# Optimization experiments

Hardware: AMD Instinct MI355X
Metric: run time of the kernel (lower is better)

The kernel has to match this reference:

```python
import jax, jax.numpy as jnp
import numpy as np

TAU = 0.03        # self.tau
EPS = 0.65       # args.epsilon
EPS2 = 0.4       # args.epsilon2 (trimap)
LOGIT_T = 0.07    # logits temperature


def _l2norm(x, axis):
    # torch F.normalize: x / max(||x||, 1e-12)
    n = jnp.sqrt(jnp.sum(x * x, axis=axis, keepdims=True))
    return x / jnp.maximum(n, 1e-12)


def setup_inputs() -> dict:
    key = jax.random.key(0)
    k1, k2 = jax.random.split(key)
    img = jax.random.normal(k1, (256, 512, 14, 14), dtype=jnp.float32)
    aud = jax.random.normal(k2, (256, 512), dtype=jnp.float32)
    return {"img": img, "aud": aud}


def reference(img, aud):
    # img: [B, C, H, W] backbone vision features; aud: [B, C] pooled audio features
    B = img.shape[0]
    img = _l2norm(img, axis=1)
    aud = _l2norm(aud, axis=1)

    # A: paired audio-visual correlation map [B, 1, H, W]
    A = jnp.einsum('nchw,nc->nhw', img, aud)[:, None]
    # A0: full cross-pair correlation maps [B, B, H, W] (n = image idx, m = audio idx)
    A0 = jnp.einsum('nchw,mc->nmhw', img, aud)
    # AdaptiveMaxPool2d((1,1)) -> max over spatial dims -> [B, B]
    A0_ref = jnp.max(A0, axis=(2, 3))

    Pos = jax.nn.sigmoid((A - EPS) / TAU)           # [B, 1, H, W]
    Pos2 = jax.nn.sigmoid((A - EPS2) / TAU)         # trimap branch
    Neg = 1.0 - Pos2
    Pos_all = jax.nn.sigmoid((A0 - EPS) / TAU)      # [B, B, H, W]

    mask = 1.0 - 100.0 * jnp.eye(B, dtype=img.dtype)
    # gated weighted-mean pooling over spatial dims
    sim = (Pos_all * A0).sum(axis=(2, 3)) / Pos_all.sum(axis=(2, 3)) * mask   # [B, B]
    sim1 = (Pos * A).sum(axis=(2, 3)) / Pos.sum(axis=(2, 3))                  # [B, 1]
    sim2 = (Neg * A).sum(axis=(2, 3)) / Neg.sum(axis=(2, 3))                  # [B, 1]

    logits = jnp.concatenate((sim1, sim, sim2), axis=1) / LOGIT_T             # [B, B+2]
    return (A, logits, Pos, Neg, A0_ref)
```

## Files before the change

### kernel.cpp

```cpp
#include <hip/hip_runtime.h>
#include <math.h>

typedef _Float16 half8 __attribute__((ext_vector_type(8)));
typedef float f32x4 __attribute__((ext_vector_type(4)));

#define RLT (1.0f/0.07f)


__device__ __forceinline__ void gll16(const void* g, void* l) {
    __builtin_amdgcn_global_load_lds(
        (const __attribute__((address_space(1))) void*)g,
        (__attribute__((address_space(3))) void*)l, 16, 0, 0);
}

__global__ __launch_bounds__(256) void prep_aud_pk(const float* __restrict__ aud,
                                                   _Float16* __restrict__ aud_pk) {
    int m = blockIdx.x, t = threadIdx.x;
    float a0 = aud[m * 512 + t];
    float a1 = aud[m * 512 + 256 + t];
    float s = a0 * a0 + a1 * a1;
    #pragma unroll
    for (int off = 32; off; off >>= 1) s += __shfl_down(s, off, 64);
    __shared__ float wsum[4];
    __shared__ float rns;
    if ((t & 63) == 0) wsum[t >> 6] = s;
    __syncthreads();
    if (t == 0) rns = 1.0f / fmaxf(sqrtf(wsum[0] + wsum[1] + wsum[2] + wsum[3]), 1e-12f);
    __syncthreads();
    float rn = rns;
    int c0 = t, c1 = t + 256;
    aud_pk[(c0 >> 3) * 2048 + m * 8 + (c0 & 7)] = (_Float16)(a0 * rn);
    aud_pk[(c1 >> 3) * 2048 + m * 8 + (c1 & 7)] = (_Float16)(a1 * rn);
}

__global__ __launch_bounds__(512) void av_mfma2(const float* __restrict__ img,
                                                const _Float16* __restrict__ aud_pk,
                                                float* __restrict__ out) {
    const int n = blockIdx.x;
    const int tid = threadIdx.x;
    const int w = tid >> 6, l = tid & 63;
    const int q = w & 3;
    const int hh = w >> 2;
    const int HT = hh ? 6 : 7;

    __shared__ _Float16 __align__(16) Abuf[2][4][208][8];
    __shared__ _Float16 __align__(16) Bbuf[2][4][256][8];
    __shared__ float rnorm_s[208];
    __shared__ float nrm_parts[2][196];
    __shared__ float red_max[2][256], red_sw[2][256], red_swa[2][256];
    __shared__ float diag_parts[2][4][4];

    if (tid < 96) {
        int b = tid / 48, rem = tid % 48, kg = rem / 12, row = 196 + rem % 12;
        *(float4*)&Abuf[b][kg][row][0] = make_float4(0.f, 0.f, 0.f, 0.f);
    }

    const float* imgn = img + (size_t)n * (512 * 196);
    const bool act = tid < 392;
    const int p   = act ? tid / 196 : 0;
    const int hws = act ? tid % 196 : 0;
    float nrm = 0.f;
    float av[16];

    #define STAGE_B(t, buf)                                                        \
        do {                                                                       \
            const _Float16* g0 = aud_pk + (((size_t)(t) * 1024 + w * 64 + l) << 3);\
            _Float16* l0 = &Bbuf[buf][0][0][0] + ((w * 64) << 3);                  \
            gll16(g0, l0);                                                         \
            gll16(g0 + 4096, l0 + 4096);                                           \
        } while (0)

    #define STAGE_A(buf)                                                           \
        do {                                                                       \
            if (act) {                                                             \
                half8 h0, h1;                                                      \
                _Pragma("unroll")                                                  \
                for (int i = 0; i < 8; i++) {                                      \
                    h0[i] = (_Float16)av[i];                                       \
                    h1[i] = (_Float16)av[8 + i];                                   \
                    nrm += av[i] * av[i] + av[8 + i] * av[8 + i];                   \
                }                                                                  \
                *(half8*)&Abuf[buf][2 * p][hws][0]     = h0;                       \
                *(half8*)&Abuf[buf][2 * p + 1][hws][0] = h1;                       \
            }                                                                      \
        } while (0)

    STAGE_B(0, 0);
    if (act) {
        const float* src = imgn + (size_t)(p * 16) * 196 + hws;
        #pragma unroll
        for (int i = 0; i < 16; i++) av[i] = src[i * 196];
    }
    STAGE_A(0);
    __syncthreads();

    f32x4 acc[7][4];
    #pragma unroll
    for (int ht = 0; ht < 7; ht++)
        #pragma unroll
        for (int mt = 0; mt < 4; mt++)
            acc[ht][mt] = (f32x4){0.f, 0.f, 0.f, 0.f};

    const int aoff = (l >> 4) * 1664 + (hh * 112 + (l & 15)) * 8;
    const int boff = (l >> 4) * 2048 + (q * 64 + (l & 15)) * 8;

    for (int t = 0; t < 16; t++) {
        const int cur = t & 1, nb = cur ^ 1;
        const bool more = t < 15;
        if (more) {
            STAGE_B(t + 1, nb);
            if (act) {
                const float* src = imgn + (size_t)(32 * (t + 1) + p * 16) * 196 + hws;
                #pragma unroll
                for (int i = 0; i < 16; i++) av[i] = src[i * 196];
            }
        }
        {
            const _Float16* Ab = &Abuf[cur][0][0][0];
            const _Float16* Bb = &Bbuf[cur][0][0][0];
            half8 bfrag[4];
            #pragma unroll
            for (int mt = 0; mt < 4; mt++) bfrag[mt] = *(const half8*)(Bb + boff + mt * 128);
            half8 afrag[7];
            #pragma unroll
            for (int ht = 0; ht < 7; ht++)
                if (ht < HT) afrag[ht] = *(const half8*)(Ab + aoff + ht * 128);
            #pragma unroll
            for (int ht = 0; ht < 7; ht++)
                if (ht < HT)
                    #pragma unroll
                    for (int mt = 0; mt < 4; mt++)
                        acc[ht][mt] = __builtin_amdgcn_mfma_f32_16x16x32_f16(
                            afrag[ht], bfrag[mt], acc[ht][mt], 0, 0, 0);
        }
        if (more) STAGE_A(nb);
        __syncthreads();
    }

    if (act) nrm_parts[p][hws] = nrm;
    __syncthreads();
    if (tid < 208) {
        float v = 0.f;
        if (tid < 196) {
            float s = nrm_parts[0][tid] + nrm_parts[1][tid];
            v = 1.0f / fmaxf(sqrtf(s), 1e-12f);
        }
        rnorm_s[tid] = v;
    }
    __syncthreads();

    float mx[4], sw[4], swa[4];
    #pragma unroll
    for (int mt = 0; mt < 4; mt++) { mx[mt] = -1e30f; sw[mt] = 0.f; swa[mt] = 0.f; }
    float s1n = 0.f, s1d = 0.f, s2n = 0.f, s2d = 0.f;
    const int dmt = (n >> 4) & 3, dq = n >> 6, dl = n & 15;
    const bool isdiag = (q == dq) && ((l & 15) == dl);

    #pragma unroll
    for (int ht = 0; ht < 7; ht++) {
        if (ht < HT) {
            int rowb = hh * 112 + ht * 16 + ((l >> 4) << 2);
            #pragma unroll
            for (int r = 0; r < 4; r++) {
                int hw = rowb + r;
                float rn = rnorm_s[hw];
                bool valid = hw < 196;
                #pragma unroll
                for (int mt = 0; mt < 4; mt++) {
                    float a0 = acc[ht][mt][r] * rn;
                    if (valid) {
                        float wg = 1.0f / (1.0f + __expf((0.65f - a0) * (1.0f / 0.03f)));
                        mx[mt]  = fmaxf(mx[mt], a0);
                        sw[mt] += wg;
                        swa[mt] += wg * a0;
                        if (isdiag && mt == dmt) {
                            out[n * 196 + hw] = a0;
                            out[116224 + n * 196 + hw] = wg;
                            float p2 = 1.0f / (1.0f + __expf((0.40f - a0) * (1.0f / 0.03f)));
                            float ng = 1.0f - p2;
                            out[166400 + n * 196 + hw] = ng;
                            s1n += wg * a0; s1d += wg;
                            s2n += ng * a0; s2d += ng;
                        }
                    }
                }
            }
        }
    }

    #pragma unroll
    for (int mt = 0; mt < 4; mt++) {
        float m1 = mx[mt], v1 = sw[mt], v2 = swa[mt];
        m1 = fmaxf(m1, __shfl_xor(m1, 16, 64)); v1 += __shfl_xor(v1, 16, 64); v2 += __shfl_xor(v2, 16, 64);
        m1 = fmaxf(m1, __shfl_xor(m1, 32, 64)); v1 += __shfl_xor(v1, 32, 64); v2 += __shfl_xor(v2, 32, 64);
        if (l < 16) {
            int m = q * 64 + mt * 16 + l;
            red_max[hh][m] = m1; red_sw[hh][m] = v1; red_swa[hh][m] = v2;
        }
    }
    if (isdiag) {
        diag_parts[hh][l >> 4][0] = s1n;
        diag_parts[hh][l >> 4][1] = s1d;
        diag_parts[hh][l >> 4][2] = s2n;
        diag_parts[hh][l >> 4][3] = s2d;
    }
    __syncthreads();

    if (tid < 256) {
        int m = tid;
        float mxv = fmaxf(red_max[0][m], red_max[1][m]);
        float num = red_swa[0][m] + red_swa[1][m];
        float den = red_sw[0][m] + red_sw[1][m];
        float sim = num / den;
        if (m == n) sim *= -99.0f;
        out[50176 + n * 258 + 1 + m] = sim * RLT;
        out[216576 + n * 256 + m] = mxv;
        if (m == n) {
            float t1n = 0.f, t1d = 0.f, t2n = 0.f, t2d = 0.f;
            #pragma unroll
            for (int h2 = 0; h2 < 2; h2++)
                #pragma unroll
                for (int g = 0; g < 4; g++) {
                    t1n += diag_parts[h2][g][0]; t1d += diag_parts[h2][g][1];
                    t2n += diag_parts[h2][g][2]; t2d += diag_parts[h2][g][3];
                }
            out[50176 + n * 258]       = (t1n / t1d) * RLT;
            out[50176 + n * 258 + 257] = (t2n / t2d) * RLT;
        }
    }
}

extern "C" void kernel_launch(void* const* d_in, const int* in_sizes, int n_in,
                              void* d_out, int out_size, void* d_ws, size_t ws_size,
                              hipStream_t stream) {
    const float* img = (const float*)d_in[0];
    const float* aud = (const float*)d_in[1];
    float* out = (float*)d_out;
    _Float16* aud_pk = (_Float16*)d_ws;

    prep_aud_pk<<<256, 256, 0, stream>>>(aud, aud_pk);
    av_mfma2<<<256, 512, 0, stream>>>(img, aud_pk, out);
}
```

Measured before the change: 48.58 us.

## Split each image's spatial range across two blocks with a separate reduction kernel

Each image is now handled by two workgroups, each covering 98 of the 196 spatial positions, so the grid grows from 256 to 512 blocks and fills more compute units on the GPU. Partial max, weighted sums and diagonal terms are written to workspace, and a new small kernel combines them to produce the logits and pooled maxima. This costs an extra kernel launch and some workspace traffic. Each block also reads the full audio tile, so B-operand staging is duplicated across the two halves.

Measured after the change: 42.78 us. 11.9% less time.

```diff
diff --git a/kernel.cpp b/kernel.cpp
--- a/kernel.cpp
+++ b/kernel.cpp
@@ -33,75 +33,84 @@
     aud_pk[(c1 >> 3) * 2048 + m * 8 + (c1 & 7)] = (_Float16)(a1 * rn);
 }
 
-__global__ __launch_bounds__(512) void av_mfma2(const float* __restrict__ img,
-                                                const _Float16* __restrict__ aud_pk,
-                                                float* __restrict__ out) {
-    const int n = blockIdx.x;
+__global__ __launch_bounds__(512, 4) void av_split(const float* __restrict__ img,
+                                                   const _Float16* __restrict__ aud_pk,
+                                                   float* __restrict__ out,
+                                                   float* __restrict__ pmax,
+                                                   float* __restrict__ psw,
+                                                   float* __restrict__ pswa,
+                                                   float* __restrict__ pdiag) {
+    const int bid = blockIdx.x;
+    const int n = bid >> 1, half = bid & 1;
     const int tid = threadIdx.x;
     const int w = tid >> 6, l = tid & 63;
     const int q = w & 3;
-    const int hh = w >> 2;
-    const int HT = hh ? 6 : 7;
-
-    __shared__ _Float16 __align__(16) Abuf[2][4][208][8];
+    const int hg = w >> 2;
+    const int HT = hg ? 3 : 4;
+
+    __shared__ _Float16 __align__(16) Abuf[2][4][112][8];
     __shared__ _Float16 __align__(16) Bbuf[2][4][256][8];
-    __shared__ float rnorm_s[208];
-    __shared__ float nrm_parts[2][196];
+    __shared__ float nrm_parts[4][98];
+    __shared__ float rnorm_s[112];
     __shared__ float red_max[2][256], red_sw[2][256], red_swa[2][256];
     __shared__ float diag_parts[2][4][4];
 
-    if (tid < 96) {
-        int b = tid / 48, rem = tid % 48, kg = rem / 12, row = 196 + rem % 12;
+    if (tid < 112) {
+        int b = tid / 56, rem = tid % 56, kg = rem / 14, row = 98 + rem % 14;
         *(float4*)&Abuf[b][kg][row][0] = make_float4(0.f, 0.f, 0.f, 0.f);
     }
 
     const float* imgn = img + (size_t)n * (512 * 196);
     const bool act = tid < 392;
-    const int p   = act ? tid / 196 : 0;
-    const int hws = act ? tid % 196 : 0;
+    const int p   = act ? tid / 98 : 0;
+    const int hwl = act ? tid % 98 : 0;
+    const int g   = half * 98 + hwl;
     float nrm = 0.f;
-    float av[16];
-
-    #define STAGE_B(t, buf)                                                        \
-        do {                                                                       \
-            const _Float16* g0 = aud_pk + (((size_t)(t) * 1024 + w * 64 + l) << 3);\
-            _Float16* l0 = &Bbuf[buf][0][0][0] + ((w * 64) << 3);                  \
-            gll16(g0, l0);                                                         \
-            gll16(g0 + 4096, l0 + 4096);                                           \
+    float av[8];
+
+    #define STAGE_B(t, buf)                                                         \
+        do {                                                                        \
+            const _Float16* g0 = aud_pk + (((size_t)(t) * 1024 + tid) << 3);        \
+            _Float16* l0 = &Bbuf[buf][0][0][0] + ((w * 64) << 3);                   \
+            gll16(g0, l0);                                                          \
+            gll16(g0 + 4096, l0 + 4096);                                            \
         } while (0)
 
-    #define STAGE_A(buf)                                                           \
-        do {                                                                       \
-            if (act) {                                                             \
-                half8 h0, h1;                                                      \
-                _Pragma("unroll")                                                  \
-                for (int i = 0; i < 8; i++) {                                      \
-                    h0[i] = (_Float16)av[i];                                       \
-                    h1[i] = (_Float16)av[8 + i];                                   \
-                    nrm += av[i] * av[i] + av[8 + i] * av[8 + i];                   \
-                }                                                                  \
-                *(half8*)&Abuf[buf][2 * p][hws][0]     = h0;                       \
-                *(half8*)&Abuf[buf][2 * p + 1][hws][0] = h1;                       \
-            }                                                                      \
+    #define LOAD_A(t)                                                               \
+        do {                                                                        \
+            if (act) {                                                              \
+                const float* src = imgn + ((size_t)(32 * (t) + p * 8)) * 196 + g;   \
+                _Pragma("unroll")                                                   \
+                for (int i = 0; i < 8; i++) av[i] = src[i * 196];                   \
+            }                                                                       \
         } while (0)
 
+    #define STAGE_A(buf)                                                            \
+        do {                                                                        \
+            if (act) {                                                              \
+                half8 h0;                                                           \
+                _Pragma("unroll")                                                   \
+                for (int i = 0; i < 8; i++) {                                       \
+                    h0[i] = (_Float16)av[i];                                        \
+                    nrm += av[i] * av[i];                                           \
+                }                                                                   \
+                *(half8*)&Abuf[buf][p][hwl][0] = h0;                                \
+            }                                                                       \
+        } while (0)
+
     STAGE_B(0, 0);
-    if (act) {
-        const float* src = imgn + (size_t)(p * 16) * 196 + hws;
-        #pragma unroll
-        for (int i = 0; i < 16; i++) av[i] = src[i * 196];
-    }
+    LOAD_A(0);
     STAGE_A(0);
     __syncthreads();
 
-    f32x4 acc[7][4];
-    #pragma unroll
-    for (int ht = 0; ht < 7; ht++)
+    f32x4 acc[4][4];
+    #pragma unroll
+    for (int ht = 0; ht < 4; ht++)
         #pragma unroll
         for (int mt = 0; mt < 4; mt++)
             acc[ht][mt] = (f32x4){0.f, 0.f, 0.f, 0.f};
 
-    const int aoff = (l >> 4) * 1664 + (hh * 112 + (l & 15)) * 8;
+    const int aoff = (l >> 4) * 896  + (hg * 64 + (l & 15)) * 8;
     const int boff = (l >> 4) * 2048 + (q * 64 + (l & 15)) * 8;
 
     for (int t = 0; t < 16; t++) {
@@ -109,11 +118,7 @@
         const bool more = t < 15;
         if (more) {
             STAGE_B(t + 1, nb);
-            if (act) {
-                const float* src = imgn + (size_t)(32 * (t + 1) + p * 16) * 196 + hws;
-                #pragma unroll
-                for (int i = 0; i < 16; i++) av[i] = src[i * 196];
-            }
+            LOAD_A(t + 1);
         }
         {
             const _Float16* Ab = &Abuf[cur][0][0][0];
@@ -121,12 +126,12 @@
             half8 bfrag[4];
             #pragma unroll
             for (int mt = 0; mt < 4; mt++) bfrag[mt] = *(const half8*)(Bb + boff + mt * 128);
-            half8 afrag[7];
-            #pragma unroll
-            for (int ht = 0; ht < 7; ht++)
+            half8 afrag[4];
+            #pragma unroll
+            for (int ht = 0; ht < 4; ht++)
                 if (ht < HT) afrag[ht] = *(const half8*)(Ab + aoff + ht * 128);
             #pragma unroll
-            for (int ht = 0; ht < 7; ht++)
+            for (int ht = 0; ht < 4; ht++)
                 if (ht < HT)
                     #pragma unroll
                     for (int mt = 0; mt < 4; mt++)
@@ -137,14 +142,13 @@
         __syncthreads();
     }
 
-    if (act) nrm_parts[p][hws] = nrm;
-    __syncthreads();
-    if (tid < 208) {
+    if (act) nrm_parts[p][hwl] = nrm;
+    __syncthreads();
+    if (tid < 112) {
         float v = 0.f;
-        if (tid < 196) {
-            float s = nrm_parts[0][tid] + nrm_parts[1][tid];
-            v = 1.0f / fmaxf(sqrtf(s), 1e-12f);
-        }
+        if (tid < 98)
+            v = 1.0f / fmaxf(sqrtf(nrm_parts[0][tid] + nrm_parts[1][tid] +
+                                   nrm_parts[2][tid] + nrm_parts[3][tid]), 1e-12f);
         rnorm_s[tid] = v;
     }
     __syncthreads();
@@ -157,14 +161,15 @@
     const bool isdiag = (q == dq) && ((l & 15) == dl);
 
     #pragma unroll
-    for (int ht = 0; ht < 7; ht++) {
+    for (int ht = 0; ht < 4; ht++) {
         if (ht < HT) {
-            int rowb = hh * 112 + ht * 16 + ((l >> 4) << 2);
+            int rowb = hg * 64 + ht * 16 + ((l >> 4) << 2);
             #pragma unroll
             for (int r = 0; r < 4; r++) {
-                int hw = rowb + r;
-                float rn = rnorm_s[hw];
-                bool valid = hw < 196;
+                int row = rowb + r;
+                float rn = rnorm_s[row];
+                bool valid = row < 98;
+                int hw = half * 98 + row;
                 #pragma unroll
                 for (int mt = 0; mt < 4; mt++) {
                     float a0 = acc[ht][mt][r] * rn;
@@ -195,38 +200,54 @@
         m1 = fmaxf(m1, __shfl_xor(m1, 32, 64)); v1 += __shfl_xor(v1, 32, 64); v2 += __shfl_xor(v2, 32, 64);
         if (l < 16) {
             int m = q * 64 + mt * 16 + l;
-            red_max[hh][m] = m1; red_sw[hh][m] = v1; red_swa[hh][m] = v2;
+            red_max[hg][m] = m1; red_sw[hg][m] = v1; red_swa[hg][m] = v2;
         }
     }
     if (isdiag) {
-        diag_parts[hh][l >> 4][0] = s1n;
-        diag_parts[hh][l >> 4][1] = s1d;
-        diag_parts[hh][l >> 4][2] = s2n;
-        diag_parts[hh][l >> 4][3] = s2d;
+        diag_parts[hg][l >> 4][0] = s1n;
+        diag_parts[hg][l >> 4][1] = s1d;
+        diag_parts[hg][l >> 4][2] = s2n;
+        diag_parts[hg][l >> 4][3] = s2d;
     }
     __syncthreads();
 
     if (tid < 256) {
         int m = tid;
-        float mxv = fmaxf(red_max[0][m], red_max[1][m]);
-        float num = red_swa[0][m] + red_swa[1][m];
-        float den = red_sw[0][m] + red_sw[1][m];
-        float sim = num / den;
-        if (m == n) sim *= -99.0f;
-        out[50176 + n * 258 + 1 + m] = sim * RLT;
-        out[216576 + n * 256 + m] = mxv;
-        if (m == n) {
-            float t1n = 0.f, t1d = 0.f, t2n = 0.f, t2d = 0.f;
-            #pragma unroll
-            for (int h2 = 0; h2 < 2; h2++)
-                #pragma unroll
-                for (int g = 0; g < 4; g++) {
-                    t1n += diag_parts[h2][g][0]; t1d += diag_parts[h2][g][1];
-                    t2n += diag_parts[h2][g][2]; t2d += diag_parts[h2][g][3];
-                }
-            out[50176 + n * 258]       = (t1n / t1d) * RLT;
-            out[50176 + n * 258 + 257] = (t2n / t2d) * RLT;
-        }
+        int base = (n * 2 + half) * 256 + m;
+        pmax[base] = fmaxf(red_max[0][m], red_max[1][m]);
+        psw[base]  = red_sw[0][m] + red_sw[1][m];
+        pswa[base] = red_swa[0][m] + red_swa[1][m];
+    }
+    if (tid < 4) {
+        float s = 0.f;
+        #pragma unroll
+        for (int h2 = 0; h2 < 2; h2++)
+            #pragma unroll
+            for (int lg = 0; lg < 4; lg++)
+                s += diag_parts[h2][lg][tid];
+        pdiag[(n * 2 + half) * 4 + tid] = s;
+    }
+    #undef STAGE_B
+    #undef LOAD_A
+    #undef STAGE_A
+}
+
+__global__ __launch_bounds__(256) void av_final(const float* __restrict__ pmax,
+                                                const float* __restrict__ psw,
+                                                const float* __restrict__ pswa,
+                                                const float* __restrict__ pdiag,
+                                                float* __restrict__ out) {
+    int n = blockIdx.x, m = threadIdx.x;
+    int b0 = (n * 2) * 256 + m, b1 = (n * 2 + 1) * 256 + m;
+    float mx = fmaxf(pmax[b0], pmax[b1]);
+    float sim = (pswa[b0] + pswa[b1]) / (psw[b0] + psw[b1]);
+    if (m == n) sim *= -99.0f;
+    out[50176 + n * 258 + 1 + m] = sim * RLT;
+    out[216576 + n * 256 + m] = mx;
+    if (m == n) {
+        const float* d = pdiag + n * 8;
+        out[50176 + n * 258]       = ((d[0] + d[4]) / (d[1] + d[5])) * RLT;
+        out[50176 + n * 258 + 257] = ((d[2] + d[6]) / (d[3] + d[7])) * RLT;
     }
 }
 
@@ -236,8 +257,15 @@
     const float* img = (const float*)d_in[0];
     const float* aud = (const float*)d_in[1];
     float* out = (float*)d_out;
+
     _Float16* aud_pk = (_Float16*)d_ws;
+    float* wsf   = (float*)d_ws;
+    float* pmax  = wsf + 32768;
+    float* psw   = pmax + 131072;
+    float* pswa  = psw + 131072;
+    float* pdiag = pswa + 131072;
 
     prep_aud_pk<<<256, 256, 0, stream>>>(aud, aud_pk);
-    av_mfma2<<<256, 512, 0, stream>>>(img, aud_pk, out);
-}
+    av_split<<<512, 512, 0, stream>>>(img, aud_pk, out, pmax, psw, pswa, pdiag);
+    av_final<<<256, 256, 0, stream>>>(pmax, psw, pswa, pdiag, out);
+}
```
